# Optimization experiments

Measured on AMD Instinct MI355X. Metric: run time of the kernel, lower is better.

## Reference

```python
import jax, jax.numpy as jnp
import numpy as np

DIM, HEADS, DH, CHUNK, DEPTH = 1024, 8, 128, 64, 2
BATCH, SEQLEN = 2, 4096
MAX_LR = 0.01
EPS = 1e-6


def _rmsnorm(x, g=None):
    y = x * jax.lax.rsqrt(jnp.mean(x * x, axis=-1, keepdims=True) + EPS)
    return y * g if g is not None else y


def _mem_mlp(ws, x):
    # MemoryMLP: x @ W0, then silu before each subsequent layer
    x = x @ ws[0]
    for w in ws[1:]:
        x = jax.nn.silu(x) @ w
    return x


def _assoc_scan(gates, x):
    # y_t = gates_t * y_{t-1} + x_t along axis 3 (chunk axis)
    g = jnp.broadcast_to(gates, x.shape)
    def op(a, b):
        ga, xa = a
        gb, xb = b
        return ga * gb, gb * xa + xb
    _, y = jax.lax.associative_scan(op, (g, x), axis=3)
    return y


def setup_inputs() -> dict:
    key = jax.random.key(0)
    ks = jax.random.split(key, 12)
    b, n, d, h, dh = BATCH, SEQLEN, DIM, HEADS, DH
    di = h * dh
    lin = lambda k, i, o: jax.random.normal(k, (i, o), jnp.float32) * np.float32(1.0 / np.sqrt(i))
    return {
        "seq": jax.random.normal(ks[0], (b, n, d), jnp.float32),
        "store_norm_g": jnp.ones((d,), jnp.float32),
        "retrieve_norm_g": jnp.ones((d,), jnp.float32),
        "w_kv": lin(ks[1], d, 2 * di),
        "w_q": lin(ks[2], d, di),
        "w_step": lin(ks[3], d, h),
        "w_mom": lin(ks[4], d, h),
        "w_decay": lin(ks[5], d, h),
        "w_gate": lin(ks[6], d, h),
        "w_combine": lin(ks[7], di, d),
        "mh_gamma": jnp.zeros((h, 1, dh), jnp.float32),
        "mem_w0": lin(ks[8], dh, dh),
        "mem_w1": lin(ks[9], dh, dh),
    }


def reference(seq, store_norm_g, retrieve_norm_g, w_kv, w_q, w_step, w_mom,
              w_decay, w_gate, w_combine, mh_gamma, mem_w0, mem_w1):
    b, n, d = seq.shape
    h, dh, c = HEADS, DH, CHUNK
    nc = n // c
    mem_ws = (mem_w0, mem_w1)

    # ---------------- store memories (chunked test-time training) ----------------
    ss = _rmsnorm(seq, store_norm_g)                                    # (b,n,d)
    lr = jax.nn.sigmoid(jnp.einsum('bnd,dh->bhn', ss, w_step)) * MAX_LR  # adaptive step
    lr = lr.reshape(b, h, nc, c)
    cmean = ss.reshape(b, nc, c, d).mean(axis=2)                        # chunk mean-reduce
    mom_gate = jax.nn.sigmoid(jnp.einsum('bnd,dh->bhn', cmean, w_mom))   # (b,h,nc)
    decay = jax.nn.sigmoid(jnp.einsum('bnd,dh->bhn', cmean, w_decay))    # (b,h,nc)

    kv = ss @ w_kv                                                      # (b,n,2*h*dh)
    keys, values = jnp.split(kv, 2, axis=-1)
    split = lambda t: t.reshape(b, n, h, dh).transpose(0, 2, 1, 3).reshape(b, h, nc, c, dh)
    keys, values = split(keys), split(values)

    # per-chunk grad of weighted mse wrt memory MLP weights (vmap(grad), as in torch.func)
    def chunk_loss(ws, k, lrc, v):
        pred = _mem_mlp(ws, k)                                          # (c,dh)
        return jnp.sum(jnp.mean((pred - v) ** 2, axis=-1) * lrc)
    flat = lambda t: t.reshape(b * h * nc, c, dh)
    grads = jax.vmap(jax.grad(chunk_loss), in_axes=(None, 0, 0, 0))(
        mem_ws, flat(keys), lr.reshape(b * h * nc, c), flat(values))
    grads = jnp.stack([g.reshape(b, h, nc, dh, dh) for g in grads])     # (depth,b,h,nc,dh,dh)
    surprise = -grads

    gm = mom_gate[None, :, :, :, None, None]
    gd = (1.0 - decay)[None, :, :, :, None, None]
    momentum = _assoc_scan(gm, surprise)                                # momentum scan over chunks
    updates = _assoc_scan(gd, momentum)                                 # decayed cumulative weight deltas

    # ---------------- retrieve memories ----------------
    sr = _rmsnorm(seq, retrieve_norm_g)
    sr = jnp.pad(sr[:, c - 1:], ((0, 0), (0, c - 1), (0, 0)))           # causal shift by chunk-1
    q = (sr @ w_q).reshape(b, n, h, dh).transpose(0, 2, 1, 3).reshape(b, h, nc, c, dh)

    w0 = mem_w0 + updates[0]                                            # (b,h,nc,dh,dh)
    w1 = mem_w1 + updates[1]
    x = jnp.einsum('bhncd,bhnde->bhnce', q, w0)
    vals = jnp.einsum('bhncd,bhnde->bhnce', jax.nn.silu(x), w1)         # (b,h,nc,c,dh)
    vals = vals.reshape(b, h, n, dh)

    vals = _rmsnorm(vals) * (mh_gamma + 1.0)                            # multihead rmsnorm
    gate = jax.nn.sigmoid(jnp.einsum('bnd,dh->bhn', sr, w_gate))[..., None]
    vals = vals * gate                                                  # retrieve gate (heads>1)
    vals = vals.transpose(0, 2, 1, 3).reshape(b, n, h * dh)             # merge heads
    out = vals @ w_combine                                              # combine heads
    out = jnp.pad(out, ((0, 0), (c - 1, 0), (0, 0)))[:, :n]             # restore alignment
    return out
```

## Files before the change

### kernel.cpp

```cpp
#include <hip/hip_runtime.h>
#include <stdint.h>


#define SEQ 4096
#define NTOK 8192

typedef unsigned short u16;
typedef __attribute__((ext_vector_type(8))) short short8;
typedef __attribute__((ext_vector_type(4))) float f32x4;
typedef __attribute__((ext_vector_type(2))) unsigned int u32x2;

__device__ __forceinline__ u16 f2b(float f) {
  union { float f; uint32_t u; } c; c.f = f;
  uint32_t u = c.u;
  uint32_t r = (u + 0x7fffu + ((u >> 16) & 1u)) >> 16;
  return (u16)r;
}
__device__ __forceinline__ float b2f(u16 h) {
  union { uint32_t u; float f; } c; c.u = ((uint32_t)h) << 16;
  return c.f;
}
__device__ __forceinline__ float sigm(float x) { return 1.f / (1.f + __expf(-x)); }
__device__ __forceinline__ uint32_t pk2(float a, float b) {
  return (uint32_t)f2b(a) | ((uint32_t)f2b(b) << 16);
}
__device__ __forceinline__ void gl16(const void* g, void* l) {
  __builtin_amdgcn_global_load_lds(
      (const __attribute__((address_space(1))) unsigned int*)g,
      (__attribute__((address_space(3))) unsigned int*)l, 16, 0, 0);
}

__device__ __forceinline__ int sidx(int r, int c) {
  return r*128 + ((((c>>3) ^ (r&7))<<3) | (c&7));
}
__device__ __forceinline__ short8 frag_row_lds128(const u16* buf, int row, int ks, int l4) {
  int g = ks*4 + l4;
  return *(const short8*)&buf[row*128 + ((g ^ (row&7))<<3)];
}
__device__ __forceinline__ short8 frag_tile(const u16* t, int row, int ks, int l4) {
  return *(const short8*)&t[row*64 + (((ks*4 + l4) ^ (row&7))<<3)];
}
__device__ __forceinline__ int taddr(int c, int r0) {
  return c*64 + (r0 ^ ((c&7)<<3));
}


__global__ __launch_bounds__(256) void prep_all(
    const float* __restrict__ wkv, const float* __restrict__ wq,
    const float* __restrict__ wcomb, const float* __restrict__ w0,
    const float* __restrict__ w1, const float* __restrict__ wstep,
    const float* __restrict__ wgatew,
    u16* __restrict__ wkvT, u16* __restrict__ wqT, u16* __restrict__ wcombT,
    u16* __restrict__ w0Ts, u16* __restrict__ w1Ts, u16* __restrict__ w1bs,
    u16* __restrict__ Bt16)
{
  __shared__ u16 tile[64*66];
  int bid = blockIdx.x;
  int tid = threadIdx.x;
  if (bid < 1024) {
    const float* src; u16* dst; int C; int bidx;
    if (bid < 512)      { src = wkv;   dst = wkvT;   C = 2048; bidx = bid; }
    else if (bid < 768) { src = wq;    dst = wqT;    C = 1024; bidx = bid - 512; }
    else                { src = wcomb; dst = wcombT; C = 1024; bidx = bid - 768; }
    const int R = 1024;
    int tiles_x = C >> 6;
    int tx = bidx % tiles_x, ty = bidx / tiles_x;
    int c0 = tx*64, r0 = ty*64;
#pragma unroll
    for (int it=0; it<16; ++it) {
      int idx = it*256 + tid;
      int rr = idx>>6, cc = idx&63;
      tile[cc*66 + rr] = f2b(src[(size_t)(r0+rr)*C + c0+cc]);
    }
    __syncthreads();
#pragma unroll
    for (int it=0; it<16; ++it) {
      int idx = it*256 + tid;
      int rr = idx>>6, cc = idx&63;
      dst[(size_t)(c0+rr)*R + r0+cc] = tile[rr*66 + cc];
    }
  } else if (bid < 1088) {
    int id = (bid-1024)*256 + tid;
    int i = id>>7, j = id&127;
    float a = w0[id], b = w1[id];
    w0Ts[sidx(j,i)] = f2b(a);
    w1Ts[sidx(j,i)] = f2b(b);
    w1bs[sidx(i,j)] = f2b(b);
  } else {
    int id = (bid-1088)*256 + tid;
    int n = id>>10, k = id&1023;
    float v = (n < 8) ? wstep[k*8 + n] : wgatew[k*8 + (n-8)];
    Bt16[id] = f2b(v);
  }
}


__global__ __launch_bounds__(256) void norms_only(
    const float* __restrict__ seq, const float* __restrict__ gs,
    const float* __restrict__ gr, u16* __restrict__ ss, u16* __restrict__ sr)
{
  int w = threadIdx.x>>6, lane = threadIdx.x&63;
  int t = blockIdx.x*4 + w;
  const float* row = seq + (size_t)t*1024;
  f32x4 x[4];
  float ssq = 0.f;
#pragma unroll
  for (int j=0;j<4;++j) {
    x[j] = *(const f32x4*)&row[j*256 + lane*4];
    ssq += x[j][0]*x[j][0] + x[j][1]*x[j][1] + x[j][2]*x[j][2] + x[j][3]*x[j][3];
  }
  for (int m=32;m;m>>=1) ssq += __shfl_xor(ssq, m);
  float inv = rsqrtf(ssq*(1.f/1024.f) + 1e-6f);
#pragma unroll
  for (int j=0;j<4;++j) {
    int d = j*256 + lane*4;
    f32x4 g4 = *(const f32x4*)&gs[d];
    f32x4 r4 = *(const f32x4*)&gr[d];
    u32x2 ps, pr;
    ps[0] = pk2(x[j][0]*inv*g4[0], x[j][1]*inv*g4[1]);
    ps[1] = pk2(x[j][2]*inv*g4[2], x[j][3]*inv*g4[3]);
    pr[0] = pk2(x[j][0]*inv*r4[0], x[j][1]*inv*r4[1]);
    pr[1] = pk2(x[j][2]*inv*r4[2], x[j][3]*inv*r4[3]);
    *(u32x2*)&ss[(size_t)t*1024 + d] = ps;
    *(u32x2*)&sr[(size_t)t*1024 + d] = pr;
  }
}


__global__ __launch_bounds__(64) void proj_kernel(
    const u16* __restrict__ ss, const u16* __restrict__ sr,
    const u16* __restrict__ Bt16, float* __restrict__ lr,
    float* __restrict__ gate)
{
  int lane = threadIdx.x;
  int l15 = lane&15, l4 = lane>>4;
  size_t t0 = (size_t)blockIdx.x*16;
  f32x4 acc1 = {}, acc2 = {};
#pragma unroll 8
  for (int ks=0; ks<32; ++ks) {
    int kof = ks*32 + l4*8;
    short8 bf = *(const short8*)&Bt16[l15*1024 + kof];
    short8 as = *(const short8*)&ss[(t0+l15)*1024 + kof];
    short8 ar = *(const short8*)&sr[(t0+l15)*1024 + kof];
    acc1 = __builtin_amdgcn_mfma_f32_16x16x32_bf16(as, bf, acc1, 0,0,0);
    acc2 = __builtin_amdgcn_mfma_f32_16x16x32_bf16(ar, bf, acc2, 0,0,0);
  }
  int col = l15;
#pragma unroll
  for (int j=0;j<4;++j) {
    int t = (int)t0 + l4*4 + j;
    int b = t>>12, pos = t&4095;
    if (col < 8) lr[((size_t)(b*8+col))*4096 + pos] = sigm(acc1[j])*0.01f;
    else gate[((size_t)(b*8+(col-8)))*4096 + pos] = sigm(acc2[j]);
  }
}


__global__ __launch_bounds__(256) void chunkgates_kernel(
    const u16* __restrict__ ss, const float* __restrict__ wmom,
    const float* __restrict__ wdec, float* __restrict__ mg,
    float* __restrict__ d1m)
{
  int bc = blockIdx.x; int b = bc>>6, ch = bc&63;
  size_t t0 = (size_t)(b*4096 + ch*64)*1024;
  int tid = threadIdx.x;
  int d0 = tid*4;
  float cm[4]; cm[0]=cm[1]=cm[2]=cm[3]=0.f;
  for (int tok=0; tok<64; ++tok) {
    u32x2 v2 = *(const u32x2*)&ss[t0 + (size_t)tok*1024 + d0];
    cm[0] += b2f((u16)(v2[0] & 0xffffu));
    cm[1] += b2f((u16)(v2[0] >> 16));
    cm[2] += b2f((u16)(v2[1] & 0xffffu));
    cm[3] += b2f((u16)(v2[1] >> 16));
  }
  float pm[8], pd[8];
#pragma unroll
  for (int h=0;h<8;++h){ pm[h]=0.f; pd[h]=0.f; }
#pragma unroll
  for (int i=0;i<4;++i) {
    float v = cm[i]*(1.f/64.f);
    int d = d0 + i;
#pragma unroll
    for (int h=0;h<8;++h){ pm[h]+=v*wmom[d*8+h]; pd[h]+=v*wdec[d*8+h]; }
  }
#pragma unroll
  for (int h=0;h<8;++h)
    for (int m=32;m;m>>=1){ pm[h] += __shfl_xor(pm[h],m); pd[h] += __shfl_xor(pd[h],m); }
  __shared__ float r2[4][16];
  int wv = tid>>6;
  if ((tid&63)==0) {
#pragma unroll
    for (int h=0;h<8;++h){ r2[wv][h]=pm[h]; r2[wv][8+h]=pd[h]; }
  }
  __syncthreads();
  if (tid < 16) {
    float s = r2[0][tid]+r2[1][tid]+r2[2][tid]+r2[3][tid];
    if (tid<8) mg[(b*8+tid)*64 + ch] = sigm(s);
    else d1m[(b*8+(tid-8))*64 + ch] = 1.f - sigm(s);
  }
}


__global__ __launch_bounds__(512, 4) void gemm_bt(
    const u16* __restrict__ A, const u16* __restrict__ Bt,
    void* __restrict__ C, int M, int N, int K, int out_f32,
    u16* __restrict__ kvT)
{
  __shared__ __align__(16) u16 As[2][128*64];
  __shared__ __align__(16) u16 Bs[2][128*64];
  int tid = threadIdx.x;
  int w = tid>>6, lane = tid&63;
  int wr = w>>2, wc = w&3;
  int l15 = lane&15, l4 = lane>>4;
  int rl = lane>>3;
  int cg = (lane&7) ^ rl;
  int nwg = gridDim.x*gridDim.y;
  int wg  = blockIdx.y*gridDim.x + blockIdx.x;
  int cpx = nwg >> 3;
  int swz = (wg & 7)*cpx + (wg >> 3);
  int bx = swz % gridDim.x, by = swz / gridDim.x;
  int brow = by*128, bcol = bx*128;
  f32x4 acc[4][2] = {};

  auto STAGE = [&](int buf, int kt) {
#pragma unroll
    for (int i=0;i<2;++i) {
      int row = w*16 + i*8;
      gl16(&A [(size_t)(brow+row+rl)*K + kt + cg*8], &As[buf][row*64]);
      gl16(&Bt[(size_t)(bcol+row+rl)*K + kt + cg*8], &Bs[buf][row*64]);
    }
  };

  int nk = K >> 6;
  STAGE(0, 0);
  asm volatile("s_waitcnt vmcnt(0)");
  __syncthreads();
  for (int t=0; t<nk; ++t) {
    int cur = t & 1;
    if (t+1 < nk) STAGE(cur^1, (t+1)*64);
#pragma unroll
    for (int ks=0; ks<2; ++ks) {
      short8 af[4], bf[2];
#pragma unroll
      for (int m=0;m<4;++m) {
        int row = wr*64 + m*16 + l15;
        int g = ks*4 + l4;
        af[m] = *(const short8*)&As[cur][row*64 + ((g ^ (row&7))<<3)];
      }
#pragma unroll
      for (int n=0;n<2;++n) {
        int row = wc*32 + n*16 + l15;
        int g = ks*4 + l4;
        bf[n] = *(const short8*)&Bs[cur][row*64 + ((g ^ (row&7))<<3)];
      }
#pragma unroll
      for (int m=0;m<4;++m)
#pragma unroll
        for (int n=0;n<2;++n)
          acc[m][n] = __builtin_amdgcn_mfma_f32_16x16x32_bf16(af[m], bf[n], acc[m][n], 0,0,0);
    }
    asm volatile("s_waitcnt vmcnt(0)");
    __syncthreads();
  }
#pragma unroll
  for (int m=0;m<4;++m) {
#pragma unroll
    for (int n=0;n<2;++n) {
      int col = bcol + wc*32 + n*16 + l15;
#pragma unroll
      for (int j=0;j<4;++j) {
        int row = brow + wr*64 + m*16 + l4*4 + j;
        if (out_f32) ((float*)C)[(size_t)row*N + col] = acc[m][n][j];
        else ((u16*)C)[(size_t)row*N + col] = f2b(acc[m][n][j]);
      }
    }
  }
  if (kvT) {
#pragma unroll
    for (int m=0;m<4;++m) {
#pragma unroll
      for (int n=0;n<2;++n) {
        int col = bcol + wc*32 + n*16 + l15;
        if (col < 1024) {
          int row0 = brow + wr*64 + m*16 + l4*4;
          int d = col & 127;
          int chunk = ((row0>>12)*8 + (col>>7))*64 + ((row0&4095)>>6);
          int rr = row0 & 63;
          u32x2 p; p[0] = pk2(acc[m][n][0], acc[m][n][1]);
                   p[1] = pk2(acc[m][n][2], acc[m][n][3]);
          *(u32x2*)&kvT[(size_t)chunk*8192 + taddr(d, rr)] = p;
        }
      }
    }
  }
}


__global__ __launch_bounds__(512) void mlp_fwd(
    const u16* __restrict__ kvout, const float* __restrict__ lr,
    const u16* __restrict__ w0Ts, const u16* __restrict__ w1Ts,
    const u16* __restrict__ w1bs,
    u16* __restrict__ aTg, u16* __restrict__ dpTg, u16* __restrict__ dxTg)
{
  __shared__ __align__(16) u16 W0L[16384];
  __shared__ __align__(16) u16 W1L[16384];
  __shared__ __align__(16) u16 WBL[16384];
  __shared__ __align__(16) u16 abuf[16384];
  int tid = threadIdx.x;
  int w = tid>>6, lane = tid&63;
  int l15 = lane&15, l4 = lane>>4;
#pragma unroll
  for (int it=0; it<4; ++it) {
    int wb = it*512 + w*64;
    gl16((const short8*)w0Ts + wb + lane, (short8*)W0L + wb);
    gl16((const short8*)w1Ts + wb + lane, (short8*)W1L + wb);
    gl16((const short8*)w1bs + wb + lane, (short8*)WBL + wb);
  }
  __syncthreads();
  u16* ab = abuf + w*2048;
  int r0 = l4*4;
  int q = w&3, half = w>>2;
  int rb = q*16;
#pragma unroll
  for (int it2=0; it2<2; ++it2) {
    int cidx = blockIdx.x*4 + it2*2 + half;
    int bh = cidx>>6, ch = cidx&63;
    int b = bh>>3, hh = bh&7;
    size_t t0 = (size_t)(b*4096 + ch*64 + rb);
    size_t tout = (size_t)cidx*8192;
    f32x4 lrv = *(const f32x4*)&lr[(size_t)bh*4096 + ch*64 + rb + r0];

    f32x4 x1[8] = {};
#pragma unroll
    for (int ks=0; ks<4; ++ks) {
      short8 af = *(const short8*)&kvout[(t0 + l15)*2048 + hh*128 + ks*32 + l4*8];
#pragma unroll
      for (int n=0;n<8;++n) {
        short8 bf = frag_row_lds128(W0L, n*16+l15, ks, l4);
        x1[n] = __builtin_amdgcn_mfma_f32_16x16x32_bf16(af, bf, x1[n], 0,0,0);
      }
    }
#pragma unroll
    for (int n=0;n<8;++n) {
      int c = n*16 + l15;
      float av[4];
#pragma unroll
      for (int j=0;j<4;++j){ float xv = x1[n][j]; av[j] = xv*sigm(xv); }
      ab[sidx(r0+0,c)] = f2b(av[0]);
      ab[sidx(r0+1,c)] = f2b(av[1]);
      ab[sidx(r0+2,c)] = f2b(av[2]);
      ab[sidx(r0+3,c)] = f2b(av[3]);
      u32x2 p; p[0] = pk2(av[0],av[1]); p[1] = pk2(av[2],av[3]);
      *(u32x2*)&aTg[tout + taddr(c, rb + r0)] = p;
    }
    f32x4 pr[8] = {};
#pragma unroll
    for (int ks=0; ks<4; ++ks) {
      short8 af = frag_row_lds128(ab, l15, ks, l4);
#pragma unroll
      for (int n=0;n<8;++n) {
        short8 bf = frag_row_lds128(W1L, n*16+l15, ks, l4);
        pr[n] = __builtin_amdgcn_mfma_f32_16x16x32_bf16(af, bf, pr[n], 0,0,0);
      }
    }
#pragma unroll
    for (int n=0;n<8;++n) {
      int c = n*16 + l15;
      float dv[4];
#pragma unroll
      for (int j=0;j<4;++j) {
        float vv = b2f(kvout[(t0+r0+j)*2048 + 1024 + hh*128 + c]);
        dv[j] = 0.015625f * lrv[j] * (pr[n][j] - vv);
      }
      ab[sidx(r0+0,c)] = f2b(dv[0]);
      ab[sidx(r0+1,c)] = f2b(dv[1]);
      ab[sidx(r0+2,c)] = f2b(dv[2]);
      ab[sidx(r0+3,c)] = f2b(dv[3]);
      u32x2 p; p[0] = pk2(dv[0],dv[1]); p[1] = pk2(dv[2],dv[3]);
      *(u32x2*)&dpTg[tout + taddr(c, rb + r0)] = p;
    }
    f32x4 da[8] = {};
#pragma unroll
    for (int ks=0; ks<4; ++ks) {
      short8 af = frag_row_lds128(ab, l15, ks, l4);
#pragma unroll
      for (int n=0;n<8;++n) {
        short8 bf = frag_row_lds128(WBL, n*16+l15, ks, l4);
        da[n] = __builtin_amdgcn_mfma_f32_16x16x32_bf16(af, bf, da[n], 0,0,0);
      }
    }
#pragma unroll
    for (int n=0;n<8;++n) {
      int c = n*16 + l15;
      float d[4];
#pragma unroll
      for (int j=0;j<4;++j) {
        float xv = x1[n][j];
        float sg = sigm(xv);
        d[j] = da[n][j]*(sg*(1.f + xv*(1.f - sg)));
      }
      u32x2 p; p[0] = pk2(d[0],d[1]); p[1] = pk2(d[2],d[3]);
      *(u32x2*)&dxTg[tout + taddr(c, rb + r0)] = p;
    }
  }
}


__global__ __launch_bounds__(256) void grad_op(
    const u16* __restrict__ dpT, const u16* __restrict__ aT,
    const u16* __restrict__ dxT, const u16* __restrict__ kT,
    u16* __restrict__ S)
{
  __shared__ __align__(16) u16 lds[16384];
  int bid = blockIdx.x;
  int op = bid >> 10;
  int sub = bid & 1023, bh = sub>>6, ch = sub&63;
  size_t tin = (size_t)sub*8192;
  const u16* Ain = op ? (dxT + tin) : (dpT + tin);
  const u16* Bin = op ? (kT  + tin) : (aT  + tin);
  int tid = threadIdx.x;
  int w = tid>>6, lane = tid&63;
  int l15 = lane&15, l4 = lane>>4;

#pragma unroll
  for (int it=0; it<4; ++it) {
    int wb = it*256 + w*64;
    gl16((const short8*)Ain + wb + lane, (short8*)lds + wb);
    gl16((const short8*)Bin + wb + lane, (short8*)(lds+8192) + wb);
  }
  __syncthreads();

  f32x4 g[2][8] = {};
#pragma unroll
  for (int ks=0; ks<2; ++ks) {
    short8 af[2];
#pragma unroll
    for (int mi=0; mi<2; ++mi)
      af[mi] = frag_tile(lds, w*32 + mi*16 + l15, ks, l4);
#pragma unroll
    for (int n=0;n<8;++n) {
      short8 bf = frag_tile(lds+8192, n*16 + l15, ks, l4);
#pragma unroll
      for (int mi=0;mi<2;++mi)
        g[mi][n] = __builtin_amdgcn_mfma_f32_16x16x32_bf16(af[mi], bf, g[mi][n], 0,0,0);
    }
  }
  __syncthreads();

#pragma unroll
  for (int mi=0;mi<2;++mi)
#pragma unroll
    for (int n=0;n<8;++n)
#pragma unroll
      for (int j=0;j<4;++j) {
        int m = w*32 + mi*16 + l4*4 + j, c = n*16 + l15;
        lds[sidx(m,c)] = f2b(-g[mi][n][j]);
      }
  __syncthreads();

  u16* Sout = S + ((size_t)((op ? bh : 16+bh))*64 + ch)*16384;
#pragma unroll
  for (int it=0; it<8; ++it)
    ((short8*)Sout)[it*256+tid] = ((const short8*)lds)[it*256+tid];
}


__global__ __launch_bounds__(256) void scan_kernel(
    u16* __restrict__ S, const float* __restrict__ mg, const float* __restrict__ d1m,
    const u16* __restrict__ w0Ts, const u16* __restrict__ w1Ts)
{
  int bidx = blockIdx.x;
  int eblk = bidx & 31;
  int mbh = bidx >> 5;
  int bh = mbh & 15;
  int e = (eblk*256 + threadIdx.x)*2;
  uint32_t* base = (uint32_t*)(S + (size_t)mbh*64*16384 + e);
  const u16* wsrc = (mbh < 16) ? w0Ts : w1Ts;
  uint32_t wp = *(const uint32_t*)&wsrc[e];
  float wv0 = b2f((u16)(wp & 0xffffu)), wv1 = b2f((u16)(wp >> 16));
  const float* g1 = mg + bh*64;
  const float* g2 = d1m + bh*64;
  float mom0=0.f, upd0=0.f, mom1=0.f, upd1=0.f;
  for (int c2=0; c2<64; ++c2) {
    uint32_t s2 = base[(size_t)c2*8192];
    float s0 = b2f((u16)(s2 & 0xffffu)), s1 = b2f((u16)(s2 >> 16));
    float gg1 = g1[c2], gg2 = g2[c2];
    mom0 = gg1*mom0 + s0; upd0 = gg2*upd0 + mom0;
    mom1 = gg1*mom1 + s1; upd1 = gg2*upd1 + mom1;
    base[(size_t)c2*8192] = pk2(wv0 + upd0, wv1 + upd1);
  }
}


__global__ __launch_bounds__(256) void retrieve_kernel(
    const u16* __restrict__ qn, const u16* __restrict__ W,
    const float* __restrict__ gamma, const float* __restrict__ gate,
    u16* __restrict__ vals)
{
  __shared__ __align__(16) u16 W0s[16384];
  __shared__ __align__(16) u16 W1s[16384];
  __shared__ __align__(16) u16 QA[8192];
  int bid = blockIdx.x;
  int bh = bid>>6, ch = bid&63;
  int b = bh>>3, h = bh&7;
  int tid = threadIdx.x;
  int w = tid>>6, lane = tid&63;
  int l15 = lane&15, l4 = lane>>4;
  const u16* W0g = W + ((size_t)bh*64 + ch)*16384;
  const u16* W1g = W + ((size_t)(16+bh)*64 + ch)*16384;
#pragma unroll
  for (int it=0; it<8; ++it) {
    int wb = it*256 + w*64;
    gl16((const short8*)W0g + wb + lane, (short8*)W0s + wb);
    gl16((const short8*)W1g + wb + lane, (short8*)W1s + wb);
  }
  if (ch == 0) {
    for (int r = w; r < 63; r += 4)
      *(uint32_t*)&vals[((size_t)(b*4096 + r))*1024 + h*128 + lane*2] = 0;
  }
  u16* qa = QA + w*2048;
#pragma unroll
  for (int it=0; it<4; ++it) {
    int task = it*64 + lane;
    int rloc = task>>4, g = task&15;
    int posn = ch*64 + w*16 + rloc + 63;
    short8 v;
    if (posn < 4096) v = *(const short8*)&qn[((size_t)(b*4096+posn))*1024 + h*128 + g*8];
    else {
#pragma unroll
      for (int i=0;i<8;++i) v[i]=0;
    }
    *(short8*)&qa[rloc*128 + ((g ^ (rloc&7))<<3)] = v;
  }
  __syncthreads();
  f32x4 xx[8] = {};
#pragma unroll
  for (int ks=0; ks<4; ++ks) {
    short8 af = frag_row_lds128(qa, l15, ks, l4);
#pragma unroll
    for (int n=0;n<8;++n) {
      short8 bf = frag_row_lds128(W0s, n*16+l15, ks, l4);
      xx[n] = __builtin_amdgcn_mfma_f32_16x16x32_bf16(af, bf, xx[n], 0,0,0);
    }
  }
  int r0 = l4*4;
#pragma unroll
  for (int n=0;n<8;++n) {
    int c = n*16 + l15;
#pragma unroll
    for (int j=0;j<4;++j) {
      float xv = xx[n][j];
      qa[sidx(r0+j,c)] = f2b(xv * sigm(xv));
    }
  }
  f32x4 vv[8] = {};
#pragma unroll
  for (int ks=0; ks<4; ++ks) {
    short8 af = frag_row_lds128(qa, l15, ks, l4);
#pragma unroll
    for (int n=0;n<8;++n) {
      short8 bf = frag_row_lds128(W1s, n*16+l15, ks, l4);
      vv[n] = __builtin_amdgcn_mfma_f32_16x16x32_bf16(af, bf, vv[n], 0,0,0);
    }
  }
#pragma unroll
  for (int j=0;j<4;++j) {
    float ssq = 0.f;
#pragma unroll
    for (int n=0;n<8;++n) ssq += vv[n][j]*vv[n][j];
    ssq += __shfl_xor(ssq,1); ssq += __shfl_xor(ssq,2);
    ssq += __shfl_xor(ssq,4); ssq += __shfl_xor(ssq,8);
    float rms = rsqrtf(ssq*(1.f/128.f) + 1e-6f);
    int posn = ch*64 + w*16 + r0 + j + 63;
    if (posn < 4096) {
      float gt = gate[(size_t)bh*4096 + posn];
      size_t orow = ((size_t)(b*4096+posn))*1024 + h*128;
#pragma unroll
      for (int n=0;n<8;++n) {
        int c = n*16 + l15;
        vals[orow + c] = f2b(vv[n][j]*rms*(1.f + gamma[h*128+c])*gt);
      }
    }
  }
}

extern "C" void kernel_launch(void* const* d_in, const int* in_sizes, int n_in,
                              void* d_out, int out_size, void* d_ws, size_t ws_size,
                              hipStream_t stream) {
  const float* seq    = (const float*)d_in[0];
  const float* gstore = (const float*)d_in[1];
  const float* gret   = (const float*)d_in[2];
  const float* wkv    = (const float*)d_in[3];
  const float* wq     = (const float*)d_in[4];
  const float* wstep  = (const float*)d_in[5];
  const float* wmom   = (const float*)d_in[6];
  const float* wdec   = (const float*)d_in[7];
  const float* wgatew = (const float*)d_in[8];
  const float* wcomb  = (const float*)d_in[9];
  const float* gamma  = (const float*)d_in[10];
  const float* w0f    = (const float*)d_in[11];
  const float* w1f    = (const float*)d_in[12];
  float* out = (float*)d_out;
  (void)in_sizes; (void)n_in; (void)out_size; (void)ws_size;

  char* p = (char*)d_ws;
  size_t off = 0;
  auto alloc = [&](size_t bytes) -> void* {
    void* r = p + off; off += (bytes + 255) & ~(size_t)255; return r;
  };
  u16* wkvT   = (u16*)alloc((size_t)2048*1024*2);
  u16* wqT    = (u16*)alloc((size_t)1024*1024*2);
  u16* wcombT = (u16*)alloc((size_t)1024*1024*2);
  u16* w0Ts   = (u16*)alloc(16384*2);
  u16* w1Ts   = (u16*)alloc(16384*2);
  u16* w1bs   = (u16*)alloc(16384*2);
  u16* Bt16   = (u16*)alloc(16384*2);
  u16* ss     = (u16*)alloc((size_t)NTOK*1024*2);
  u16* sr     = (u16*)alloc((size_t)NTOK*1024*2);
  u16* kvout  = (u16*)alloc((size_t)NTOK*2048*2);
  u16* qn     = (u16*)alloc((size_t)NTOK*1024*2);
  u16* vals   = (u16*)alloc((size_t)NTOK*1024*2);
  float* lr   = (float*)alloc((size_t)16*4096*4);
  float* gate = (float*)alloc((size_t)16*4096*4);
  float* mg   = (float*)alloc(1024*4);
  float* d1m  = (float*)alloc(1024*4);
  u16* S      = (u16*)alloc((size_t)32*64*16384*2);
  u16* kTg    = (u16*)alloc((size_t)1024*8192*2);
  u16* aTg    = (u16*)alloc((size_t)1024*8192*2);
  u16* dpTg   = (u16*)alloc((size_t)1024*8192*2);
  u16* dxTg   = (u16*)alloc((size_t)1024*8192*2);

  prep_all<<<dim3(1152),dim3(256),0,stream>>>(wkv, wq, wcomb, w0f, w1f, wstep, wgatew,
                                              wkvT, wqT, wcombT, w0Ts, w1Ts, w1bs, Bt16);
  norms_only<<<dim3(2048),dim3(256),0,stream>>>(seq, gstore, gret, ss, sr);
  proj_kernel<<<dim3(512),dim3(64),0,stream>>>(ss, sr, Bt16, lr, gate);
  chunkgates_kernel<<<dim3(128),dim3(256),0,stream>>>(ss, wmom, wdec, mg, d1m);
  gemm_bt<<<dim3(16,64),dim3(512),0,stream>>>(ss, wkvT, kvout, 8192, 2048, 1024, 0, kTg);
  gemm_bt<<<dim3(8,64),dim3(512),0,stream>>>(sr, wqT, qn, 8192, 1024, 1024, 0, nullptr);
  mlp_fwd<<<dim3(256),dim3(512),0,stream>>>(kvout, lr, w0Ts, w1Ts, w1bs, aTg, dpTg, dxTg);
  grad_op<<<dim3(2048),dim3(256),0,stream>>>(dpTg, aTg, dxTg, kTg, S);
  scan_kernel<<<dim3(1024),dim3(256),0,stream>>>(S, mg, d1m, w0Ts, w1Ts);
  retrieve_kernel<<<dim3(1024),dim3(256),0,stream>>>(qn, S, gamma, gate, vals);
  gemm_bt<<<dim3(8,64),dim3(512),0,stream>>>(vals, wcombT, out, 8192, 1024, 1024, 1, nullptr);
}
```

Baseline: 226.6 us.

## Use 4-wave GEMM tiles and shrink mlp_fwd LDS by reading W1 from global

The bf16 GEMM now runs 256 threads per block. Each wave computes a 64x64 sub-tile with 4x4 MFMA accumulators and stages 4 rows per load, which doubles per-wave register reuse and halves the wave count. mlp_fwd processes one chunk per half-block instead of two, with twice as many blocks. It also drops the two W1 LDS copies and reads W1 fragments directly from global/L2 in plain row-major layouts, cutting LDS use to raise occupancy. The risks are higher GEMM register pressure, lower latency hiding with fewer waves, and unstaged global reads inside the MFMA loops.

```diff
diff --git a/kernel.cpp b/kernel.cpp
--- a/kernel.cpp
+++ b/kernel.cpp
@@ -51,8 +51,8 @@
     const float* __restrict__ w1, const float* __restrict__ wstep,
     const float* __restrict__ wgatew,
     u16* __restrict__ wkvT, u16* __restrict__ wqT, u16* __restrict__ wcombT,
-    u16* __restrict__ w0Ts, u16* __restrict__ w1Ts, u16* __restrict__ w1bs,
-    u16* __restrict__ Bt16)
+    u16* __restrict__ w0Ts, u16* __restrict__ w1Ts, u16* __restrict__ w1Tp,
+    u16* __restrict__ w1bp, u16* __restrict__ Bt16)
 {
   __shared__ u16 tile[64*66];
   int bid = blockIdx.x;
@@ -85,7 +85,8 @@
     float a = w0[id], b = w1[id];
     w0Ts[sidx(j,i)] = f2b(a);
     w1Ts[sidx(j,i)] = f2b(b);
-    w1bs[sidx(i,j)] = f2b(b);
+    w1Tp[j*128+i] = f2b(b);
+    w1bp[id] = f2b(b);
   } else {
     int id = (bid-1088)*256 + tid;
     int n = id>>10, k = id&1023;
@@ -201,7 +202,7 @@
 }
 
 
-__global__ __launch_bounds__(512, 4) void gemm_bt(
+__global__ __launch_bounds__(256, 2) void gemm_bt(
     const u16* __restrict__ A, const u16* __restrict__ Bt,
     void* __restrict__ C, int M, int N, int K, int out_f32,
     u16* __restrict__ kvT)
@@ -210,7 +211,7 @@
   __shared__ __align__(16) u16 Bs[2][128*64];
   int tid = threadIdx.x;
   int w = tid>>6, lane = tid&63;
-  int wr = w>>2, wc = w&3;
+  int wr = w>>1, wc = w&1;
   int l15 = lane&15, l4 = lane>>4;
   int rl = lane>>3;
   int cg = (lane&7) ^ rl;
@@ -220,12 +221,12 @@
   int swz = (wg & 7)*cpx + (wg >> 3);
   int bx = swz % gridDim.x, by = swz / gridDim.x;
   int brow = by*128, bcol = bx*128;
-  f32x4 acc[4][2] = {};
+  f32x4 acc[4][4] = {};
 
   auto STAGE = [&](int buf, int kt) {
 #pragma unroll
-    for (int i=0;i<2;++i) {
-      int row = w*16 + i*8;
+    for (int i=0;i<4;++i) {
+      int row = w*32 + i*8;
       gl16(&A [(size_t)(brow+row+rl)*K + kt + cg*8], &As[buf][row*64]);
       gl16(&Bt[(size_t)(bcol+row+rl)*K + kt + cg*8], &Bs[buf][row*64]);
     }
@@ -240,7 +241,7 @@
     if (t+1 < nk) STAGE(cur^1, (t+1)*64);
 #pragma unroll
     for (int ks=0; ks<2; ++ks) {
-      short8 af[4], bf[2];
+      short8 af[4], bf[4];
 #pragma unroll
       for (int m=0;m<4;++m) {
         int row = wr*64 + m*16 + l15;
@@ -248,15 +249,15 @@
         af[m] = *(const short8*)&As[cur][row*64 + ((g ^ (row&7))<<3)];
       }
 #pragma unroll
-      for (int n=0;n<2;++n) {
-        int row = wc*32 + n*16 + l15;
+      for (int n=0;n<4;++n) {
+        int row = wc*64 + n*16 + l15;
         int g = ks*4 + l4;
         bf[n] = *(const short8*)&Bs[cur][row*64 + ((g ^ (row&7))<<3)];
       }
 #pragma unroll
       for (int m=0;m<4;++m)
 #pragma unroll
-        for (int n=0;n<2;++n)
+        for (int n=0;n<4;++n)
           acc[m][n] = __builtin_amdgcn_mfma_f32_16x16x32_bf16(af[m], bf[n], acc[m][n], 0,0,0);
     }
     asm volatile("s_waitcnt vmcnt(0)");
@@ -265,8 +266,8 @@
 #pragma unroll
   for (int m=0;m<4;++m) {
 #pragma unroll
-    for (int n=0;n<2;++n) {
-      int col = bcol + wc*32 + n*16 + l15;
+    for (int n=0;n<4;++n) {
+      int col = bcol + wc*64 + n*16 + l15;
 #pragma unroll
       for (int j=0;j<4;++j) {
         int row = brow + wr*64 + m*16 + l4*4 + j;
@@ -279,8 +280,8 @@
 #pragma unroll
     for (int m=0;m<4;++m) {
 #pragma unroll
-      for (int n=0;n<2;++n) {
-        int col = bcol + wc*32 + n*16 + l15;
+      for (int n=0;n<4;++n) {
+        int col = bcol + wc*64 + n*16 + l15;
         if (col < 1024) {
           int row0 = brow + wr*64 + m*16 + l4*4;
           int d = col & 127;
@@ -298,13 +299,11 @@
 
 __global__ __launch_bounds__(512) void mlp_fwd(
     const u16* __restrict__ kvout, const float* __restrict__ lr,
-    const u16* __restrict__ w0Ts, const u16* __restrict__ w1Ts,
-    const u16* __restrict__ w1bs,
+    const u16* __restrict__ w0Ts, const u16* __restrict__ w1Tp,
+    const u16* __restrict__ w1bp,
     u16* __restrict__ aTg, u16* __restrict__ dpTg, u16* __restrict__ dxTg)
 {
   __shared__ __align__(16) u16 W0L[16384];
-  __shared__ __align__(16) u16 W1L[16384];
-  __shared__ __align__(16) u16 WBL[16384];
   __shared__ __align__(16) u16 abuf[16384];
   int tid = threadIdx.x;
   int w = tid>>6, lane = tid&63;
@@ -313,95 +312,92 @@
   for (int it=0; it<4; ++it) {
     int wb = it*512 + w*64;
     gl16((const short8*)w0Ts + wb + lane, (short8*)W0L + wb);
-    gl16((const short8*)w1Ts + wb + lane, (short8*)W1L + wb);
-    gl16((const short8*)w1bs + wb + lane, (short8*)WBL + wb);
   }
   __syncthreads();
   u16* ab = abuf + w*2048;
   int r0 = l4*4;
   int q = w&3, half = w>>2;
   int rb = q*16;
-#pragma unroll
-  for (int it2=0; it2<2; ++it2) {
-    int cidx = blockIdx.x*4 + it2*2 + half;
-    int bh = cidx>>6, ch = cidx&63;
-    int b = bh>>3, hh = bh&7;
-    size_t t0 = (size_t)(b*4096 + ch*64 + rb);
-    size_t tout = (size_t)cidx*8192;
-    f32x4 lrv = *(const f32x4*)&lr[(size_t)bh*4096 + ch*64 + rb + r0];
-
-    f32x4 x1[8] = {};
-#pragma unroll
-    for (int ks=0; ks<4; ++ks) {
-      short8 af = *(const short8*)&kvout[(t0 + l15)*2048 + hh*128 + ks*32 + l4*8];
-#pragma unroll
-      for (int n=0;n<8;++n) {
-        short8 bf = frag_row_lds128(W0L, n*16+l15, ks, l4);
-        x1[n] = __builtin_amdgcn_mfma_f32_16x16x32_bf16(af, bf, x1[n], 0,0,0);
-      }
-    }
+  int cidx = blockIdx.x*2 + half;
+  int bh = cidx>>6, ch = cidx&63;
+  int b = bh>>3, hh = bh&7;
+  size_t t0 = (size_t)(b*4096 + ch*64 + rb);
+  size_t tout = (size_t)cidx*8192;
+  f32x4 lrv = *(const f32x4*)&lr[(size_t)bh*4096 + ch*64 + rb + r0];
+
+  f32x4 x1[8] = {};
+#pragma unroll
+  for (int ks=0; ks<4; ++ks) {
+    short8 af = *(const short8*)&kvout[(t0 + l15)*2048 + hh*128 + ks*32 + l4*8];
 #pragma unroll
     for (int n=0;n<8;++n) {
-      int c = n*16 + l15;
-      float av[4];
-#pragma unroll
-      for (int j=0;j<4;++j){ float xv = x1[n][j]; av[j] = xv*sigm(xv); }
-      ab[sidx(r0+0,c)] = f2b(av[0]);
-      ab[sidx(r0+1,c)] = f2b(av[1]);
-      ab[sidx(r0+2,c)] = f2b(av[2]);
-      ab[sidx(r0+3,c)] = f2b(av[3]);
-      u32x2 p; p[0] = pk2(av[0],av[1]); p[1] = pk2(av[2],av[3]);
-      *(u32x2*)&aTg[tout + taddr(c, rb + r0)] = p;
-    }
-    f32x4 pr[8] = {};
-#pragma unroll
-    for (int ks=0; ks<4; ++ks) {
-      short8 af = frag_row_lds128(ab, l15, ks, l4);
-#pragma unroll
-      for (int n=0;n<8;++n) {
-        short8 bf = frag_row_lds128(W1L, n*16+l15, ks, l4);
-        pr[n] = __builtin_amdgcn_mfma_f32_16x16x32_bf16(af, bf, pr[n], 0,0,0);
-      }
-    }
+      short8 bf = frag_row_lds128(W0L, n*16+l15, ks, l4);
+      x1[n] = __builtin_amdgcn_mfma_f32_16x16x32_bf16(af, bf, x1[n], 0,0,0);
+    }
+  }
+#pragma unroll
+  for (int n=0;n<8;++n) {
+    int c = n*16 + l15;
+    float av[4];
+#pragma unroll
+    for (int j=0;j<4;++j){ float xv = x1[n][j]; av[j] = xv*sigm(xv); }
+    ab[sidx(r0+0,c)] = f2b(av[0]);
+    ab[sidx(r0+1,c)] = f2b(av[1]);
+    ab[sidx(r0+2,c)] = f2b(av[2]);
+    ab[sidx(r0+3,c)] = f2b(av[3]);
+    u32x2 p; p[0] = pk2(av[0],av[1]); p[1] = pk2(av[2],av[3]);
+    *(u32x2*)&aTg[tout + taddr(c, rb + r0)] = p;
+  }
+  f32x4 pr[8] = {};
+#pragma unroll
+  for (int ks=0; ks<4; ++ks) {
+    short8 af = frag_row_lds128(ab, l15, ks, l4);
+    int kof = ks*32 + l4*8;
 #pragma unroll
     for (int n=0;n<8;++n) {
-      int c = n*16 + l15;
-      float dv[4];
-#pragma unroll
-      for (int j=0;j<4;++j) {
-        float vv = b2f(kvout[(t0+r0+j)*2048 + 1024 + hh*128 + c]);
-        dv[j] = 0.015625f * lrv[j] * (pr[n][j] - vv);
-      }
-      ab[sidx(r0+0,c)] = f2b(dv[0]);
-      ab[sidx(r0+1,c)] = f2b(dv[1]);
-      ab[sidx(r0+2,c)] = f2b(dv[2]);
-      ab[sidx(r0+3,c)] = f2b(dv[3]);
-      u32x2 p; p[0] = pk2(dv[0],dv[1]); p[1] = pk2(dv[2],dv[3]);
-      *(u32x2*)&dpTg[tout + taddr(c, rb + r0)] = p;
-    }
-    f32x4 da[8] = {};
-#pragma unroll
-    for (int ks=0; ks<4; ++ks) {
-      short8 af = frag_row_lds128(ab, l15, ks, l4);
-#pragma unroll
-      for (int n=0;n<8;++n) {
-        short8 bf = frag_row_lds128(WBL, n*16+l15, ks, l4);
-        da[n] = __builtin_amdgcn_mfma_f32_16x16x32_bf16(af, bf, da[n], 0,0,0);
-      }
-    }
+      short8 bf = *(const short8*)&w1Tp[(size_t)(n*16+l15)*128 + kof];
+      pr[n] = __builtin_amdgcn_mfma_f32_16x16x32_bf16(af, bf, pr[n], 0,0,0);
+    }
+  }
+#pragma unroll
+  for (int n=0;n<8;++n) {
+    int c = n*16 + l15;
+    float dv[4];
+#pragma unroll
+    for (int j=0;j<4;++j) {
+      float vv = b2f(kvout[(t0+r0+j)*2048 + 1024 + hh*128 + c]);
+      dv[j] = 0.015625f * lrv[j] * (pr[n][j] - vv);
+    }
+    ab[sidx(r0+0,c)] = f2b(dv[0]);
+    ab[sidx(r0+1,c)] = f2b(dv[1]);
+    ab[sidx(r0+2,c)] = f2b(dv[2]);
+    ab[sidx(r0+3,c)] = f2b(dv[3]);
+    u32x2 p; p[0] = pk2(dv[0],dv[1]); p[1] = pk2(dv[2],dv[3]);
+    *(u32x2*)&dpTg[tout + taddr(c, rb + r0)] = p;
+  }
+  f32x4 da[8] = {};
+#pragma unroll
+  for (int ks=0; ks<4; ++ks) {
+    short8 af = frag_row_lds128(ab, l15, ks, l4);
+    int kof = ks*32 + l4*8;
 #pragma unroll
     for (int n=0;n<8;++n) {
-      int c = n*16 + l15;
-      float d[4];
-#pragma unroll
-      for (int j=0;j<4;++j) {
-        float xv = x1[n][j];
-        float sg = sigm(xv);
-        d[j] = da[n][j]*(sg*(1.f + xv*(1.f - sg)));
-      }
-      u32x2 p; p[0] = pk2(d[0],d[1]); p[1] = pk2(d[2],d[3]);
-      *(u32x2*)&dxTg[tout + taddr(c, rb + r0)] = p;
-    }
+      short8 bf = *(const short8*)&w1bp[(size_t)(n*16+l15)*128 + kof];
+      da[n] = __builtin_amdgcn_mfma_f32_16x16x32_bf16(af, bf, da[n], 0,0,0);
+    }
+  }
+#pragma unroll
+  for (int n=0;n<8;++n) {
+    int c = n*16 + l15;
+    float d[4];
+#pragma unroll
+    for (int j=0;j<4;++j) {
+      float xv = x1[n][j];
+      float sg = sigm(xv);
+      d[j] = da[n][j]*(sg*(1.f + xv*(1.f - sg)));
+    }
+    u32x2 p; p[0] = pk2(d[0],d[1]); p[1] = pk2(d[2],d[3]);
+    *(u32x2*)&dxTg[tout + taddr(c, rb + r0)] = p;
   }
 }
 
@@ -613,7 +609,8 @@
   u16* wcombT = (u16*)alloc((size_t)1024*1024*2);
   u16* w0Ts   = (u16*)alloc(16384*2);
   u16* w1Ts   = (u16*)alloc(16384*2);
-  u16* w1bs   = (u16*)alloc(16384*2);
+  u16* w1Tp   = (u16*)alloc(16384*2);
+  u16* w1bp   = (u16*)alloc(16384*2);
   u16* Bt16   = (u16*)alloc(16384*2);
   u16* ss     = (u16*)alloc((size_t)NTOK*1024*2);
   u16* sr     = (u16*)alloc((size_t)NTOK*1024*2);
@@ -631,15 +628,15 @@
   u16* dxTg   = (u16*)alloc((size_t)1024*8192*2);
 
   prep_all<<<dim3(1152),dim3(256),0,stream>>>(wkv, wq, wcomb, w0f, w1f, wstep, wgatew,
-                                              wkvT, wqT, wcombT, w0Ts, w1Ts, w1bs, Bt16);
+                                              wkvT, wqT, wcombT, w0Ts, w1Ts, w1Tp, w1bp, Bt16);
   norms_only<<<dim3(2048),dim3(256),0,stream>>>(seq, gstore, gret, ss, sr);
   proj_kernel<<<dim3(512),dim3(64),0,stream>>>(ss, sr, Bt16, lr, gate);
   chunkgates_kernel<<<dim3(128),dim3(256),0,stream>>>(ss, wmom, wdec, mg, d1m);
-  gemm_bt<<<dim3(16,64),dim3(512),0,stream>>>(ss, wkvT, kvout, 8192, 2048, 1024, 0, kTg);
-  gemm_bt<<<dim3(8,64),dim3(512),0,stream>>>(sr, wqT, qn, 8192, 1024, 1024, 0, nullptr);
-  mlp_fwd<<<dim3(256),dim3(512),0,stream>>>(kvout, lr, w0Ts, w1Ts, w1bs, aTg, dpTg, dxTg);
+  gemm_bt<<<dim3(16,64),dim3(256),0,stream>>>(ss, wkvT, kvout, 8192, 2048, 1024, 0, kTg);
+  gemm_bt<<<dim3(8,64),dim3(256),0,stream>>>(sr, wqT, qn, 8192, 1024, 1024, 0, nullptr);
+  mlp_fwd<<<dim3(512),dim3(512),0,stream>>>(kvout, lr, w0Ts, w1Tp, w1bp, aTg, dpTg, dxTg);
   grad_op<<<dim3(2048),dim3(256),0,stream>>>(dpTg, aTg, dxTg, kTg, S);
   scan_kernel<<<dim3(1024),dim3(256),0,stream>>>(S, mg, d1m, w0Ts, w1Ts);
   retrieve_kernel<<<dim3(1024),dim3(256),0,stream>>>(qn, S, gamma, gate, vals);
-  gemm_bt<<<dim3(8,64),dim3(512),0,stream>>>(vals, wcombT, out, 8192, 1024, 1024, 1, nullptr);
-}
+  gemm_bt<<<dim3(8,64),dim3(256),0,stream>>>(vals, wcombT, out, 8192, 1024, 1024, 1, nullptr);
+}
```

Result: slower. 258.0 us (+13.9%).
